# Optimization experiments

Measured on AMD Instinct MI355X. Metric: run time of the kernel, lower is better.

The kernel has to match this reference:

```python
import jax, jax.numpy as jnp
import numpy as np

FRAME_NUMBER = 1200

def _relgcn(x, W, rows, cols, vals, n_nodes):
    # Multi-relation sparse GCN: sum_r A_r @ (x @ W_r), then tanh.
    out = jnp.zeros((n_nodes, W.shape[-1]), dtype=x.dtype)
    for r in range(W.shape[0]):  # fixed small set of relations (5)
        xl = x @ W[r]                              # [N, D]
        msgs = vals[r][:, None] * xl[cols[r]]      # [E, D] gather
        out = out + jax.ops.segment_sum(msgs, rows[r], num_segments=n_nodes)
    return jnp.tanh(out)

def setup_inputs() -> dict:
    key = jax.random.key(0)
    ks = jax.random.split(key, 20)
    N, E, R, D, B, C = 11201, 100000, 5, 512, 32, 16
    s = lambda k, sh, sc=0.05: jax.random.normal(k, sh, dtype=jnp.float32) * sc
    return {
        "target_span": jax.random.normal(ks[0], (B, 4 * 512), dtype=jnp.float32),
        "frame_emb": s(ks[1], (FRAME_NUMBER + 1, D), 1.0),
        "role_emb": s(ks[2], (10001, D), 1.0),
        "rel_W0": s(ks[3], (R, D, D)),
        "rel_W1": s(ks[4], (R, D, D)),
        "span_W1": s(ks[5], (2048, 2048)),
        "span_b1": s(ks[6], (2048,)),
        "span_W2": s(ks[7], (2048, D)),
        "span_b2": s(ks[8], (D,)),
        "fp_W1": s(ks[9], (D, D)),
        "fp_b1": s(ks[10], (D,)),
        "fp_W2": s(ks[11], (D, D)),
        "fp_b2": s(ks[12], (D,)),
        "adj_vals": jax.random.uniform(ks[13], (R, E), dtype=jnp.float32),
        "fe_ids": jax.random.randint(ks[14], (10001,), 0, 10001),
        "adj_rows": jax.random.randint(ks[15], (R, E), 0, N),
        "adj_cols": jax.random.randint(ks[16], (R, E), 0, N),
        "gold_frame_id": jax.random.randint(ks[17], (B,), 0, C),
        "frame_list": jax.random.randint(ks[18], (B, C), 0, FRAME_NUMBER),
    }

def reference(target_span, frame_emb, role_emb, rel_W0, rel_W1,
              span_W1, span_b1, span_W2, span_b2,
              fp_W1, fp_b1, fp_W2, fp_b2, adj_vals,
              fe_ids, adj_rows, adj_cols, gold_frame_id, frame_list):
    B = target_span.shape[0]
    # Embedding lookups (frame_embedding(arange(frame_number)), role_embedding(fe_dict ids))
    all_frame = frame_emb[:FRAME_NUMBER]            # [1200, D]
    all_fe = role_emb[fe_ids]                       # [10001, D]
    x = jnp.concatenate([all_frame, all_fe], axis=0)  # [N, D]
    N = x.shape[0]
    # Two-layer multi-relation GCN over 5 sparse adjacencies
    x = _relgcn(x, rel_W0, adj_rows, adj_cols, adj_vals, N)
    all_embeddings = _relgcn(x, rel_W1, adj_rows, adj_cols, adj_vals, N)  # [N, D]
    # span_fc_layer Mlp: Linear(2048,2048) -> ReLU -> Linear(2048,512) (dropout in eval = identity)
    target_node = jax.nn.relu(target_span @ span_W1 + span_b1) @ span_W2 + span_b2  # [B, D]
    # frame_pred = RoleClassification: Linear -> ReLU -> Linear -> Tanh, then bmm with all node embeddings
    Q = jnp.tanh(jax.nn.relu(target_node @ fp_W1 + fp_b1) @ fp_W2 + fp_b2)          # [B, D]
    pred_frame_weight = jnp.einsum("nd,bd->bn", all_embeddings, Q)[:, :FRAME_NUMBER]  # [B, 1200]
    # gold frame path: one-hot select gold frame id from candidates, gather its node embedding
    gold_frame_label = jnp.take_along_axis(frame_list, gold_frame_id[:, None], axis=1)[:, 0]  # [B]
    frame_node = all_embeddings[gold_frame_label]   # [B, D] (embed_dropout in eval = identity)
    return jnp.concatenate([pred_frame_weight, frame_node], axis=-1)  # [B, 1200+512]
```

## Files before the change

kernel.cpp:

```cpp
#include <hip/hip_runtime.h>
#include <hip/hip_bf16.h>
#include <stdint.h>

typedef unsigned short u16;
typedef __attribute__((ext_vector_type(8))) short short8;
typedef __attribute__((ext_vector_type(4))) float float4v;

#define NNODES 11201
#define MPAD   11264
#define EEDGES 100000
#define RREL   5
#define DDIM   512
#define XLW    2560
#define FRAMES 1200
#define OUTC   1712

__device__ __forceinline__ float bf2f(u16 h) {
    return __uint_as_float(((uint32_t)h) << 16);
}
__device__ __forceinline__ u16 f2bf(float f) {
    uint32_t x = __float_as_uint(f);
    x += 0x7fffu + ((x >> 16) & 1u);
    return (u16)(x >> 16);
}
__device__ __forceinline__ float fast_tanh(float v) {
    v = fminf(fmaxf(v, -10.f), 10.f);
    float ex = __expf(2.f * v);
    return (ex - 1.f) / (ex + 1.f);
}

__global__ void hist_k(const int* __restrict__ rows, int* __restrict__ counts) {
    int tid = blockIdx.x * 256 + threadIdx.x;
    if (tid >= RREL * EEDGES) return;
    int r = tid / EEDGES;
    atomicAdd(&counts[r * NNODES + rows[tid]], 1);
}

__global__ __launch_bounds__(1024) void scan_offsets(const int* __restrict__ counts,
                                                     int* __restrict__ offs) {
    int r = blockIdx.x;
    const int* c = counts + (size_t)r * NNODES;
    int* o = offs + (size_t)r * (NNODES + 1);
    __shared__ int wsum[16];
    __shared__ int carry_s;
    const int lane = threadIdx.x & 63, wid = threadIdx.x >> 6;
    if (threadIdx.x == 0) carry_s = 0;
    __syncthreads();
    for (int base = 0; base < NNODES; base += 1024) {
        int idx = base + threadIdx.x;
        int orig = (idx < NNODES) ? c[idx] : 0;
        int v = orig;
        #pragma unroll
        for (int d = 1; d < 64; d <<= 1) {
            int t = __shfl_up(v, d, 64);
            if (lane >= d) v += t;
        }
        if (lane == 63) wsum[wid] = v;
        __syncthreads();
        if (wid == 0) {
            int wv = (lane < 16) ? wsum[lane] : 0;
            #pragma unroll
            for (int d = 1; d < 16; d <<= 1) {
                int t = __shfl_up(wv, d, 64);
                if (lane >= d) wv += t;
            }
            if (lane < 16) wsum[lane] = wv;
        }
        __syncthreads();
        int incl = carry_s + ((wid > 0) ? wsum[wid - 1] : 0) + v;
        if (idx < NNODES) o[idx] = incl - orig;
        __syncthreads();
        if (threadIdx.x == 1023) carry_s = incl;
    }
    __syncthreads();
    if (threadIdx.x == 0) o[NNODES] = carry_s;
}

__global__ void cursor_init(const int* __restrict__ offs, int* __restrict__ cursor) {
    int i = blockIdx.x * 256 + threadIdx.x;
    if (i >= RREL * NNODES) return;
    int r = i / NNODES, n = i - r * NNODES;
    cursor[i] = offs[r * (NNODES + 1) + n];
}

__global__ void scatter_k(const int* __restrict__ rows, const int* __restrict__ cols,
                          const float* __restrict__ vals, int* __restrict__ cursor,
                          int* __restrict__ colS, float* __restrict__ valS) {
    int tid = blockIdx.x * 256 + threadIdx.x;
    if (tid >= RREL * EEDGES) return;
    int r = tid / EEDGES;
    int row = rows[tid];
    int pos = atomicAdd(&cursor[r * NNODES + row], 1);
    colS[(size_t)r * EEDGES + pos] = cols[tid];
    valS[(size_t)r * EEDGES + pos] = vals[tid];
}

__global__ void build_x(const float* __restrict__ frame_emb, const float* __restrict__ role_emb,
                        const int* __restrict__ fe_ids, u16* __restrict__ x) {
    int t = blockIdx.x * 256 + threadIdx.x;
    int row = t >> 7, c4 = (t & 127) << 2;
    if (row >= NNODES) return;
    const float* src = (row < FRAMES) ? (frame_emb + (size_t)row * DDIM)
                                      : (role_emb + (size_t)fe_ids[row - FRAMES] * DDIM);
    float4 v = *(const float4*)(src + c4);
    ushort4 o = { f2bf(v.x), f2bf(v.y), f2bf(v.z), f2bf(v.w) };
    *(ushort4*)(x + (size_t)row * DDIM + c4) = o;
}

__global__ void build_tsp(const float* __restrict__ ts, u16* __restrict__ tsp) {
    int t = blockIdx.x * 256 + threadIdx.x;
    int row = t >> 9, c4 = (t & 511) << 2;
    ushort4 o = {0, 0, 0, 0};
    if (row < 32) {
        float4 v = *(const float4*)(ts + (size_t)row * 2048 + c4);
        o = ushort4{ f2bf(v.x), f2bf(v.y), f2bf(v.z), f2bf(v.w) };
    }
    *(ushort4*)(tsp + (size_t)row * 2048 + c4) = o;
}

__global__ void transpose_f2b(const float* __restrict__ in, u16* __restrict__ out,
                              int rows, int cols, int ldOut) {
    __shared__ u16 tile[32][33];
    in += (size_t)blockIdx.z * rows * cols;
    const size_t zoff = (size_t)blockIdx.z * rows;
    int c0 = blockIdx.x * 32, r0 = blockIdx.y * 32;
    int tx = threadIdx.x & 31, ty = threadIdx.x >> 5;
    #pragma unroll
    for (int i = 0; i < 4; ++i) {
        int rr = ty + i * 8;
        tile[rr][tx] = f2bf(in[(size_t)(r0 + rr) * cols + c0 + tx]);
    }
    __syncthreads();
    #pragma unroll
    for (int i = 0; i < 4; ++i) {
        int rr = ty + i * 8;
        out[(size_t)(c0 + rr) * ldOut + zoff + r0 + tx] = tile[tx][rr];
    }
}

template<int EPI, bool FOUT>
__global__ __launch_bounds__(256)
void gemm_bt(const u16* __restrict__ A, const u16* __restrict__ Bt,
             void* __restrict__ Cv, const float* __restrict__ bias,
             int K, int lda, int ldb, int ldc, int mGuard, int nGuard)
{
    __shared__ u16 As[128 * 32];
    __shared__ u16 Bs[128 * 32];
    const int tid = threadIdx.x;
    const int wave = tid >> 6, lane = tid & 63;
    const int m0 = blockIdx.y * 128, n0 = blockIdx.x * 128;
    const int srow = lane >> 2;
    const int skoff = (lane & 3) << 3;
    const int fr = lane & 15, quad = lane >> 4;
    const int wm = (wave & 1) << 6, wn = (wave >> 1) << 6;
    float4v acc[4][4] = {};

    for (int k0 = 0; k0 < K; k0 += 32) {
        #pragma unroll
        for (int i = 0; i < 2; ++i) {
            const int rb = (wave + i * 4) << 4;
            const u16* ga = A  + (size_t)(m0 + rb + srow) * lda + (k0 + skoff);
            const u16* gb = Bt + (size_t)(n0 + rb + srow) * ldb + (k0 + skoff);
            __builtin_amdgcn_global_load_lds(
                (const __attribute__((address_space(1))) unsigned int*)ga,
                (__attribute__((address_space(3))) unsigned int*)(As + rb * 32), 16, 0, 0);
            __builtin_amdgcn_global_load_lds(
                (const __attribute__((address_space(1))) unsigned int*)gb,
                (__attribute__((address_space(3))) unsigned int*)(Bs + rb * 32), 16, 0, 0);
        }
        __syncthreads();
        short8 a[4], b[4];
        #pragma unroll
        for (int t = 0; t < 4; ++t)
            a[t] = *(const short8*)(As + ((wm + t * 16 + fr) << 5) + (quad << 3));
        #pragma unroll
        for (int t = 0; t < 4; ++t)
            b[t] = *(const short8*)(Bs + ((wn + t * 16 + fr) << 5) + (quad << 3));
        #pragma unroll
        for (int i = 0; i < 4; ++i)
            #pragma unroll
            for (int j = 0; j < 4; ++j)
                acc[i][j] = __builtin_amdgcn_mfma_f32_16x16x32_bf16(a[i], b[j], acc[i][j], 0, 0, 0);
        __syncthreads();
    }

    #pragma unroll
    for (int i = 0; i < 4; ++i) {
        #pragma unroll
        for (int j = 0; j < 4; ++j) {
            const int n = n0 + wn + j * 16 + fr;
            float bv = 0.f;
            if (EPI == 1 || EPI == 2 || EPI == 3) { if (n < nGuard) bv = bias[n]; }
            #pragma unroll
            for (int rg = 0; rg < 4; ++rg) {
                const int m = m0 + wm + i * 16 + (quad << 2) + rg;
                if (m < mGuard && n < nGuard) {
                    float v = acc[i][j][rg];
                    if (EPI == 1 || EPI == 2 || EPI == 3) v += bv;
                    if (EPI == 1) v = fmaxf(v, 0.f);
                    if (EPI == 3 || EPI == 4) v = fast_tanh(v);
                    if (FOUT) ((float*)Cv)[(size_t)m * ldc + n] = v;
                    else      ((u16*)Cv)[(size_t)m * ldc + n] = f2bf(v);
                }
            }
        }
    }
}

__global__ __launch_bounds__(256)
void gemm_bt_sk(const u16* __restrict__ A, const u16* __restrict__ Bt,
                float* __restrict__ Cf, int K, int Kc, int lda, int ldb, int ldc)
{
    __shared__ u16 As[128 * 32];
    __shared__ u16 Bs[128 * 32];
    const int tid = threadIdx.x;
    const int wave = tid >> 6, lane = tid & 63;
    const int m0 = blockIdx.y * 128, n0 = blockIdx.x * 128;
    const int kb = blockIdx.z * Kc;
    const int ke = (kb + Kc < K) ? (kb + Kc) : K;
    const int srow = lane >> 2;
    const int skoff = (lane & 3) << 3;
    const int fr = lane & 15, quad = lane >> 4;
    const int wm = (wave & 1) << 6, wn = (wave >> 1) << 6;
    float4v acc[4][4] = {};

    for (int k0 = kb; k0 < ke; k0 += 32) {
        #pragma unroll
        for (int i = 0; i < 2; ++i) {
            const int rb = (wave + i * 4) << 4;
            const u16* ga = A  + (size_t)(m0 + rb + srow) * lda + (k0 + skoff);
            const u16* gb = Bt + (size_t)(n0 + rb + srow) * ldb + (k0 + skoff);
            __builtin_amdgcn_global_load_lds(
                (const __attribute__((address_space(1))) unsigned int*)ga,
                (__attribute__((address_space(3))) unsigned int*)(As + rb * 32), 16, 0, 0);
            __builtin_amdgcn_global_load_lds(
                (const __attribute__((address_space(1))) unsigned int*)gb,
                (__attribute__((address_space(3))) unsigned int*)(Bs + rb * 32), 16, 0, 0);
        }
        __syncthreads();
        short8 a[4], b[4];
        #pragma unroll
        for (int t = 0; t < 4; ++t)
            a[t] = *(const short8*)(As + ((wm + t * 16 + fr) << 5) + (quad << 3));
        #pragma unroll
        for (int t = 0; t < 4; ++t)
            b[t] = *(const short8*)(Bs + ((wn + t * 16 + fr) << 5) + (quad << 3));
        #pragma unroll
        for (int i = 0; i < 4; ++i)
            #pragma unroll
            for (int j = 0; j < 4; ++j)
                acc[i][j] = __builtin_amdgcn_mfma_f32_16x16x32_bf16(a[i], b[j], acc[i][j], 0, 0, 0);
        __syncthreads();
    }

    #pragma unroll
    for (int i = 0; i < 4; ++i)
        #pragma unroll
        for (int j = 0; j < 4; ++j) {
            const int n = n0 + wn + j * 16 + fr;
            #pragma unroll
            for (int rg = 0; rg < 4; ++rg) {
                const int m = m0 + wm + i * 16 + (quad << 2) + rg;
                atomicAdd(&Cf[(size_t)m * ldc + n], acc[i][j][rg]);
            }
        }
}

template<int ACT>
__global__ void sk_ep(const float* __restrict__ Cf, const float* __restrict__ bias,
                      u16* __restrict__ outp, int Ncols) {
    int t = blockIdx.x * 256 + threadIdx.x;
    if (t >= 128 * Ncols / 4) return;
    int i = t << 2;
    int col = i & (Ncols - 1);
    float4 v = *(const float4*)(Cf + i);
    v.x += bias[col]; v.y += bias[col + 1]; v.z += bias[col + 2]; v.w += bias[col + 3];
    if (ACT == 1) { v.x = fmaxf(v.x, 0.f); v.y = fmaxf(v.y, 0.f);
                    v.z = fmaxf(v.z, 0.f); v.w = fmaxf(v.w, 0.f); }
    if (ACT == 3) { v.x = fast_tanh(v.x); v.y = fast_tanh(v.y);
                    v.z = fast_tanh(v.z); v.w = fast_tanh(v.w); }
    ushort4 o = { f2bf(v.x), f2bf(v.y), f2bf(v.z), f2bf(v.w) };
    *(ushort4*)(outp + i) = o;
}

__device__ __forceinline__ void fma8(float* acc, uint4 u, float val) {
    acc[0] = fmaf(val, __uint_as_float(u.x << 16), acc[0]);
    acc[1] = fmaf(val, __uint_as_float(u.x & 0xffff0000u), acc[1]);
    acc[2] = fmaf(val, __uint_as_float(u.y << 16), acc[2]);
    acc[3] = fmaf(val, __uint_as_float(u.y & 0xffff0000u), acc[3]);
    acc[4] = fmaf(val, __uint_as_float(u.z << 16), acc[4]);
    acc[5] = fmaf(val, __uint_as_float(u.z & 0xffff0000u), acc[5]);
    acc[6] = fmaf(val, __uint_as_float(u.w << 16), acc[6]);
    acc[7] = fmaf(val, __uint_as_float(u.w & 0xffff0000u), acc[7]);
}

__global__ __launch_bounds__(256)
void spmm_agg(const u16* __restrict__ x, const int* __restrict__ offs,
              const int* __restrict__ colS, const float* __restrict__ valS,
              u16* __restrict__ agg)
{
    const int wave = threadIdx.x >> 6, lane = threadIdx.x & 63;
    const int n = blockIdx.x * 4 + wave;
    if (n >= NNODES) return;
    const u16* xr = x + (lane << 3);
    #pragma unroll
    for (int r = 0; r < RREL; ++r) {
        int s = offs[r * (NNODES + 1) + n];
        const int e = offs[r * (NNODES + 1) + n + 1];
        const int*   cp = colS + (size_t)r * EEDGES;
        const float* vp = valS + (size_t)r * EEDGES;
        float acc[8] = {0.f, 0.f, 0.f, 0.f, 0.f, 0.f, 0.f, 0.f};
        for (; s + 4 <= e; s += 4) {
            int   c0 = cp[s], c1 = cp[s + 1], c2 = cp[s + 2], c3 = cp[s + 3];
            float v0 = vp[s], v1 = vp[s + 1], v2 = vp[s + 2], v3 = vp[s + 3];
            uint4 u0 = *(const uint4*)(xr + (size_t)c0 * DDIM);
            uint4 u1 = *(const uint4*)(xr + (size_t)c1 * DDIM);
            uint4 u2 = *(const uint4*)(xr + (size_t)c2 * DDIM);
            uint4 u3 = *(const uint4*)(xr + (size_t)c3 * DDIM);
            fma8(acc, u0, v0); fma8(acc, u1, v1); fma8(acc, u2, v2); fma8(acc, u3, v3);
        }
        for (; s < e; ++s) {
            int col = cp[s];
            float val = vp[s];
            uint4 u = *(const uint4*)(xr + (size_t)col * DDIM);
            fma8(acc, u, val);
        }
        uint4 o;
        o.x = (uint32_t)f2bf(acc[0]) | ((uint32_t)f2bf(acc[1]) << 16);
        o.y = (uint32_t)f2bf(acc[2]) | ((uint32_t)f2bf(acc[3]) << 16);
        o.z = (uint32_t)f2bf(acc[4]) | ((uint32_t)f2bf(acc[5]) << 16);
        o.w = (uint32_t)f2bf(acc[6]) | ((uint32_t)f2bf(acc[7]) << 16);
        *(uint4*)(agg + (size_t)n * XLW + (r << 9) + (lane << 3)) = o;
    }
}

__global__ void frame_gather(const u16* __restrict__ emb, const int* __restrict__ frame_list,
                             const int* __restrict__ gold, float* __restrict__ out) {
    int t = blockIdx.x * 256 + threadIdx.x;
    if (t >= 32 * 64) return;
    int b = t >> 6, lane = t & 63;
    int label = frame_list[b * 16 + gold[b]];
    const u16* src = emb + (size_t)label * DDIM + (lane << 3);
    float* dst = out + (size_t)b * OUTC + FRAMES + (lane << 3);
    float4 o0 = { bf2f(src[0]), bf2f(src[1]), bf2f(src[2]), bf2f(src[3]) };
    float4 o1 = { bf2f(src[4]), bf2f(src[5]), bf2f(src[6]), bf2f(src[7]) };
    *(float4*)(dst) = o0;
    *(float4*)(dst + 4) = o1;
}

extern "C" void kernel_launch(void* const* d_in, const int* in_sizes, int n_in,
                              void* d_out, int out_size, void* d_ws, size_t ws_size,
                              hipStream_t stream) {
    const float* target_span = (const float*)d_in[0];
    const float* frame_emb   = (const float*)d_in[1];
    const float* role_emb    = (const float*)d_in[2];
    const float* rel_W0      = (const float*)d_in[3];
    const float* rel_W1      = (const float*)d_in[4];
    const float* span_W1     = (const float*)d_in[5];
    const float* span_b1     = (const float*)d_in[6];
    const float* span_W2     = (const float*)d_in[7];
    const float* span_b2     = (const float*)d_in[8];
    const float* fp_W1       = (const float*)d_in[9];
    const float* fp_b1       = (const float*)d_in[10];
    const float* fp_W2       = (const float*)d_in[11];
    const float* fp_b2       = (const float*)d_in[12];
    const float* adj_vals    = (const float*)d_in[13];
    const int* fe_ids      = (const int*)d_in[14];
    const int* adj_rows    = (const int*)d_in[15];
    const int* adj_cols    = (const int*)d_in[16];
    const int* gold_id     = (const int*)d_in[17];
    const int* frame_list  = (const int*)d_in[18];
    float* out = (float*)d_out;

    char* ws = (char*)d_ws;
    size_t off = 0;
    auto take = [&](size_t bytes) -> char* {
        char* p = ws + off;
        off = (off + bytes + 255) & ~(size_t)255;
        return p;
    };
    u16* x      = (u16*)take((size_t)MPAD * DDIM * 2);
    u16* agg    = (u16*)take((size_t)MPAD * XLW * 2);
    u16* w0t    = (u16*)take((size_t)512 * XLW * 2);
    u16* w1t    = (u16*)take((size_t)512 * XLW * 2);
    u16* s1t    = (u16*)take((size_t)2048 * 2048 * 2);
    u16* s2t    = (u16*)take((size_t)512 * 2048 * 2);
    u16* f1t    = (u16*)take((size_t)512 * 512 * 2);
    u16* f2t    = (u16*)take((size_t)512 * 512 * 2);
    int* counts = (int*)take((size_t)RREL * NNODES * 4);
    int* offs   = (int*)take((size_t)RREL * (NNODES + 1) * 4);
    int* cursor = (int*)take((size_t)RREL * NNODES * 4);
    int* colS   = (int*)take((size_t)RREL * EEDGES * 4);
    float* valS = (float*)take((size_t)RREL * EEDGES * 4);
    u16* tsp    = (u16*)take((size_t)128 * 2048 * 2);
    u16* h1     = (u16*)take((size_t)128 * 2048 * 2);
    u16* tn     = (u16*)take((size_t)128 * 512 * 2);
    u16* h2     = (u16*)take((size_t)128 * 512 * 2);
    u16* Qb     = (u16*)take((size_t)128 * 512 * 2);
    float* CfAll = (float*)take((size_t)(128 * 2048 + 3 * 128 * 512) * 4);
    float* Cf1 = CfAll;
    float* Cf2 = Cf1 + 128 * 2048;
    float* Cf3 = Cf2 + 128 * 512;
    float* Cf4 = Cf3 + 128 * 512;

    hipMemsetAsync(counts, 0, (size_t)RREL * NNODES * 4, stream);
    hipMemsetAsync(CfAll, 0, (size_t)(128 * 2048 + 3 * 128 * 512) * 4, stream);

    hist_k<<<(RREL * EEDGES + 255) / 256, 256, 0, stream>>>(adj_rows, counts);
    scan_offsets<<<RREL, 1024, 0, stream>>>(counts, offs);
    cursor_init<<<(RREL * NNODES + 255) / 256, 256, 0, stream>>>(offs, cursor);
    scatter_k<<<(RREL * EEDGES + 255) / 256, 256, 0, stream>>>(adj_rows, adj_cols, adj_vals,
                                                               cursor, colS, valS);
    build_x<<<(NNODES * 128 + 255) / 256, 256, 0, stream>>>(frame_emb, role_emb, fe_ids, x);
    build_tsp<<<256, 256, 0, stream>>>(target_span, tsp);

    transpose_f2b<<<dim3(16, 16, RREL), 256, 0, stream>>>(rel_W0, w0t, 512, 512, XLW);
    transpose_f2b<<<dim3(16, 16, RREL), 256, 0, stream>>>(rel_W1, w1t, 512, 512, XLW);
    transpose_f2b<<<dim3(64, 64, 1), 256, 0, stream>>>(span_W1, s1t, 2048, 2048, 2048);
    transpose_f2b<<<dim3(16, 64, 1), 256, 0, stream>>>(span_W2, s2t, 2048, 512, 2048);
    transpose_f2b<<<dim3(16, 16, 1), 256, 0, stream>>>(fp_W1, f1t, 512, 512, 512);
    transpose_f2b<<<dim3(16, 16, 1), 256, 0, stream>>>(fp_W2, f2t, 512, 512, 512);

    spmm_agg<<<(NNODES + 3) / 4, 256, 0, stream>>>(x, offs, colS, valS, agg);
    gemm_bt<4, false><<<dim3(4, MPAD / 128), 256, 0, stream>>>(
        agg, w0t, x, nullptr, XLW, XLW, XLW, 512, NNODES, 512);
    spmm_agg<<<(NNODES + 3) / 4, 256, 0, stream>>>(x, offs, colS, valS, agg);
    gemm_bt<4, false><<<dim3(4, MPAD / 128), 256, 0, stream>>>(
        agg, w1t, x, nullptr, XLW, XLW, XLW, 512, NNODES, 512);

    gemm_bt_sk<<<dim3(16, 1, 8), 256, 0, stream>>>(tsp, s1t, Cf1, 2048, 256, 2048, 2048, 2048);
    sk_ep<1><<<(128 * 2048 / 4 + 255) / 256, 256, 0, stream>>>(Cf1, span_b1, h1, 2048);
    gemm_bt_sk<<<dim3(4, 1, 8), 256, 0, stream>>>(h1, s2t, Cf2, 2048, 256, 2048, 2048, 512);
    sk_ep<2><<<(128 * 512 / 4 + 255) / 256, 256, 0, stream>>>(Cf2, span_b2, tn, 512);
    gemm_bt_sk<<<dim3(4, 1, 4), 256, 0, stream>>>(tn, f1t, Cf3, 512, 128, 512, 512, 512);
    sk_ep<1><<<(128 * 512 / 4 + 255) / 256, 256, 0, stream>>>(Cf3, fp_b1, h2, 512);
    gemm_bt_sk<<<dim3(4, 1, 4), 256, 0, stream>>>(h2, f2t, Cf4, 512, 128, 512, 512, 512);
    sk_ep<3><<<(128 * 512 / 4 + 255) / 256, 256, 0, stream>>>(Cf4, fp_b2, Qb, 512);

    gemm_bt<0, true><<<dim3((FRAMES + 127) / 128, 1), 256, 0, stream>>>(
        Qb, x, out, nullptr, 512, 512, 512, OUTC, 32, FRAMES);
    frame_gather<<<8, 256, 0, stream>>>(x, frame_list, gold_id, out);
}
```

Baseline: 546.2 us.

## Split-K the GCN GEMMs, swizzle LDS reads, and merge small prep kernels

The two large GCN GEMMs (M=11264, K=2560) now use split-K over 5 slices, accumulating with atomics into an fp32 buffer followed by a separate tanh epilogue pass. The final prediction GEMM is also split-K. The LDS load offsets are XOR-swizzled to reduce bank conflicts, and the offset scan now computes each relation in a single pass and writes the cursors directly. The embedding, span, and weight conversion kernels are merged into two launches. In exchange, this adds a 23MB fp32 buffer with extra memsets and an epilogue pass per layer, and float atomics make the accumulation order nondeterministic.

```diff
diff --git a/kernel.cpp b/kernel.cpp
--- a/kernel.cpp
+++ b/kernel.cpp
@@ -37,50 +37,50 @@
 }
 
 __global__ __launch_bounds__(1024) void scan_offsets(const int* __restrict__ counts,
-                                                     int* __restrict__ offs) {
+                                                     int* __restrict__ offs,
+                                                     int* __restrict__ cursor) {
+    const int PER = 11;
     int r = blockIdx.x;
     const int* c = counts + (size_t)r * NNODES;
     int* o = offs + (size_t)r * (NNODES + 1);
+    int* cur = cursor + (size_t)r * NNODES;
     __shared__ int wsum[16];
-    __shared__ int carry_s;
     const int lane = threadIdx.x & 63, wid = threadIdx.x >> 6;
-    if (threadIdx.x == 0) carry_s = 0;
+    int base = threadIdx.x * PER;
+    int v[PER];
+    int s = 0;
+    #pragma unroll
+    for (int t = 0; t < PER; ++t) {
+        int idx = base + t;
+        v[t] = (idx < NNODES) ? c[idx] : 0;
+        s += v[t];
+    }
+    int incl = s;
+    #pragma unroll
+    for (int d = 1; d < 64; d <<= 1) {
+        int t = __shfl_up(incl, d, 64);
+        if (lane >= d) incl += t;
+    }
+    if (lane == 63) wsum[wid] = incl;
     __syncthreads();
-    for (int base = 0; base < NNODES; base += 1024) {
-        int idx = base + threadIdx.x;
-        int orig = (idx < NNODES) ? c[idx] : 0;
-        int v = orig;
-        #pragma unroll
-        for (int d = 1; d < 64; d <<= 1) {
-            int t = __shfl_up(v, d, 64);
-            if (lane >= d) v += t;
-        }
-        if (lane == 63) wsum[wid] = v;
-        __syncthreads();
-        if (wid == 0) {
-            int wv = (lane < 16) ? wsum[lane] : 0;
-            #pragma unroll
-            for (int d = 1; d < 16; d <<= 1) {
-                int t = __shfl_up(wv, d, 64);
-                if (lane >= d) wv += t;
-            }
-            if (lane < 16) wsum[lane] = wv;
-        }
-        __syncthreads();
-        int incl = carry_s + ((wid > 0) ? wsum[wid - 1] : 0) + v;
-        if (idx < NNODES) o[idx] = incl - orig;
-        __syncthreads();
-        if (threadIdx.x == 1023) carry_s = incl;
+    if (wid == 0) {
+        int wv = (lane < 16) ? wsum[lane] : 0;
+        #pragma unroll
+        for (int d = 1; d < 16; d <<= 1) {
+            int t = __shfl_up(wv, d, 64);
+            if (lane >= d) wv += t;
+        }
+        if (lane < 16) wsum[lane] = wv;
     }
     __syncthreads();
-    if (threadIdx.x == 0) o[NNODES] = carry_s;
-}
-
-__global__ void cursor_init(const int* __restrict__ offs, int* __restrict__ cursor) {
-    int i = blockIdx.x * 256 + threadIdx.x;
-    if (i >= RREL * NNODES) return;
-    int r = i / NNODES, n = i - r * NNODES;
-    cursor[i] = offs[r * (NNODES + 1) + n];
+    int run = incl - s + ((wid > 0) ? wsum[wid - 1] : 0);
+    #pragma unroll
+    for (int t = 0; t < PER; ++t) {
+        int idx = base + t;
+        if (idx < NNODES) { o[idx] = run; cur[idx] = run; }
+        run += v[t];
+    }
+    if (threadIdx.x == 1023) o[NNODES] = run;
 }
 
 __global__ void scatter_k(const int* __restrict__ rows, const int* __restrict__ cols,
@@ -95,67 +95,109 @@
     valS[(size_t)r * EEDGES + pos] = vals[tid];
 }
 
-__global__ void build_x(const float* __restrict__ frame_emb, const float* __restrict__ role_emb,
-                        const int* __restrict__ fe_ids, u16* __restrict__ x) {
-    int t = blockIdx.x * 256 + threadIdx.x;
-    int row = t >> 7, c4 = (t & 127) << 2;
-    if (row >= NNODES) return;
-    const float* src = (row < FRAMES) ? (frame_emb + (size_t)row * DDIM)
-                                      : (role_emb + (size_t)fe_ids[row - FRAMES] * DDIM);
-    float4 v = *(const float4*)(src + c4);
-    ushort4 o = { f2bf(v.x), f2bf(v.y), f2bf(v.z), f2bf(v.w) };
-    *(ushort4*)(x + (size_t)row * DDIM + c4) = o;
-}
-
-__global__ void build_tsp(const float* __restrict__ ts, u16* __restrict__ tsp) {
-    int t = blockIdx.x * 256 + threadIdx.x;
-    int row = t >> 9, c4 = (t & 511) << 2;
-    ushort4 o = {0, 0, 0, 0};
-    if (row < 32) {
-        float4 v = *(const float4*)(ts + (size_t)row * 2048 + c4);
-        o = ushort4{ f2bf(v.x), f2bf(v.y), f2bf(v.z), f2bf(v.w) };
-    }
-    *(ushort4*)(tsp + (size_t)row * 2048 + c4) = o;
-}
-
-__global__ void transpose_f2b(const float* __restrict__ in, u16* __restrict__ out,
-                              int rows, int cols, int ldOut) {
+#define BX_BLOCKS 5601
+__global__ void prep_inputs(const float* __restrict__ frame_emb,
+                            const float* __restrict__ role_emb,
+                            const int* __restrict__ fe_ids,
+                            const float* __restrict__ ts,
+                            u16* __restrict__ x, u16* __restrict__ tsp) {
+    int bid = blockIdx.x;
+    if (bid < BX_BLOCKS) {
+        int t = bid * 256 + threadIdx.x;
+        int row = t >> 7, c4 = (t & 127) << 2;
+        if (row >= NNODES) return;
+        const float* src = (row < FRAMES) ? (frame_emb + (size_t)row * DDIM)
+                                          : (role_emb + (size_t)fe_ids[row - FRAMES] * DDIM);
+        float4 v = *(const float4*)(src + c4);
+        ushort4 o = { f2bf(v.x), f2bf(v.y), f2bf(v.z), f2bf(v.w) };
+        *(ushort4*)(x + (size_t)row * DDIM + c4) = o;
+    } else {
+        int t = (bid - BX_BLOCKS) * 256 + threadIdx.x;
+        int row = t >> 9, c4 = (t & 511) << 2;
+        ushort4 o = {0, 0, 0, 0};
+        if (row < 32) {
+            float4 v = *(const float4*)(ts + (size_t)row * 2048 + c4);
+            o = ushort4{ f2bf(v.x), f2bf(v.y), f2bf(v.z), f2bf(v.w) };
+        }
+        *(ushort4*)(tsp + (size_t)row * 2048 + c4) = o;
+    }
+}
+
+__global__ void transpose_all(const float* __restrict__ w0, const float* __restrict__ w1,
+                              const float* __restrict__ s1, const float* __restrict__ s2,
+                              const float* __restrict__ f1, const float* __restrict__ f2,
+                              u16* __restrict__ w0t, u16* __restrict__ w1t,
+                              u16* __restrict__ s1t, u16* __restrict__ s2t,
+                              u16* __restrict__ f1t, u16* __restrict__ f2t) {
+    int b = blockIdx.x;
+    const float* src; u16* dst;
+    int cols, ldOut, bx, by;
+    size_t zcol = 0;
+    if (b < 1280) {
+        int rel = b >> 8, rem = b & 255;
+        src = w0 + (size_t)rel * 262144; dst = w0t;
+        cols = 512; ldOut = XLW; zcol = (size_t)rel * 512;
+        bx = rem & 15; by = rem >> 4;
+    } else if (b < 2560) {
+        b -= 1280;
+        int rel = b >> 8, rem = b & 255;
+        src = w1 + (size_t)rel * 262144; dst = w1t;
+        cols = 512; ldOut = XLW; zcol = (size_t)rel * 512;
+        bx = rem & 15; by = rem >> 4;
+    } else if (b < 6656) {
+        b -= 2560;
+        src = s1; dst = s1t; cols = 2048; ldOut = 2048;
+        bx = b & 63; by = b >> 6;
+    } else if (b < 7680) {
+        b -= 6656;
+        src = s2; dst = s2t; cols = 512; ldOut = 2048;
+        bx = b & 15; by = b >> 4;
+    } else if (b < 7936) {
+        b -= 7680;
+        src = f1; dst = f1t; cols = 512; ldOut = 512;
+        bx = b & 15; by = b >> 4;
+    } else {
+        b -= 7936;
+        src = f2; dst = f2t; cols = 512; ldOut = 512;
+        bx = b & 15; by = b >> 4;
+    }
     __shared__ u16 tile[32][33];
-    in += (size_t)blockIdx.z * rows * cols;
-    const size_t zoff = (size_t)blockIdx.z * rows;
-    int c0 = blockIdx.x * 32, r0 = blockIdx.y * 32;
+    int c0 = bx * 32, r0 = by * 32;
     int tx = threadIdx.x & 31, ty = threadIdx.x >> 5;
     #pragma unroll
     for (int i = 0; i < 4; ++i) {
         int rr = ty + i * 8;
-        tile[rr][tx] = f2bf(in[(size_t)(r0 + rr) * cols + c0 + tx]);
+        tile[rr][tx] = f2bf(src[(size_t)(r0 + rr) * cols + c0 + tx]);
     }
     __syncthreads();
     #pragma unroll
     for (int i = 0; i < 4; ++i) {
         int rr = ty + i * 8;
-        out[(size_t)(c0 + rr) * ldOut + zoff + r0 + tx] = tile[tx][rr];
-    }
-}
-
-template<int EPI, bool FOUT>
+        dst[(size_t)(c0 + rr) * ldOut + zcol + r0 + tx] = tile[tx][rr];
+    }
+}
+
+template<bool GUARDM>
 __global__ __launch_bounds__(256)
-void gemm_bt(const u16* __restrict__ A, const u16* __restrict__ Bt,
-             void* __restrict__ Cv, const float* __restrict__ bias,
-             int K, int lda, int ldb, int ldc, int mGuard, int nGuard)
+void gemm_sk(const u16* __restrict__ A, const u16* __restrict__ Bt,
+             float* __restrict__ Cf, int K, int Kc,
+             int lda, int ldb, int ldc, int mGuard)
 {
     __shared__ u16 As[128 * 32];
     __shared__ u16 Bs[128 * 32];
     const int tid = threadIdx.x;
     const int wave = tid >> 6, lane = tid & 63;
     const int m0 = blockIdx.y * 128, n0 = blockIdx.x * 128;
+    const int kb = blockIdx.z * Kc;
     const int srow = lane >> 2;
-    const int skoff = (lane & 3) << 3;
+    const int schunk = ((lane & 3) - (lane >> 4)) & 3;
+    const int skoff = schunk << 3;
     const int fr = lane & 15, quad = lane >> 4;
+    const int pa = ((quad + (fr >> 2)) & 3) << 3;
     const int wm = (wave & 1) << 6, wn = (wave >> 1) << 6;
     float4v acc[4][4] = {};
 
-    for (int k0 = 0; k0 < K; k0 += 32) {
+    for (int k0 = kb; k0 < kb + Kc; k0 += 32) {
         #pragma unroll
         for (int i = 0; i < 2; ++i) {
             const int rb = (wave + i * 4) << 4;
@@ -172,10 +214,10 @@
         short8 a[4], b[4];
         #pragma unroll
         for (int t = 0; t < 4; ++t)
-            a[t] = *(const short8*)(As + ((wm + t * 16 + fr) << 5) + (quad << 3));
+            a[t] = *(const short8*)(As + ((wm + t * 16 + fr) << 5) + pa);
         #pragma unroll
         for (int t = 0; t < 4; ++t)
-            b[t] = *(const short8*)(Bs + ((wn + t * 16 + fr) << 5) + (quad << 3));
+            b[t] = *(const short8*)(Bs + ((wn + t * 16 + fr) << 5) + pa);
         #pragma unroll
         for (int i = 0; i < 4; ++i)
             #pragma unroll
@@ -185,75 +227,6 @@
     }
 
     #pragma unroll
-    for (int i = 0; i < 4; ++i) {
-        #pragma unroll
-        for (int j = 0; j < 4; ++j) {
-            const int n = n0 + wn + j * 16 + fr;
-            float bv = 0.f;
-            if (EPI == 1 || EPI == 2 || EPI == 3) { if (n < nGuard) bv = bias[n]; }
-            #pragma unroll
-            for (int rg = 0; rg < 4; ++rg) {
-                const int m = m0 + wm + i * 16 + (quad << 2) + rg;
-                if (m < mGuard && n < nGuard) {
-                    float v = acc[i][j][rg];
-                    if (EPI == 1 || EPI == 2 || EPI == 3) v += bv;
-                    if (EPI == 1) v = fmaxf(v, 0.f);
-                    if (EPI == 3 || EPI == 4) v = fast_tanh(v);
-                    if (FOUT) ((float*)Cv)[(size_t)m * ldc + n] = v;
-                    else      ((u16*)Cv)[(size_t)m * ldc + n] = f2bf(v);
-                }
-            }
-        }
-    }
-}
-
-__global__ __launch_bounds__(256)
-void gemm_bt_sk(const u16* __restrict__ A, const u16* __restrict__ Bt,
-                float* __restrict__ Cf, int K, int Kc, int lda, int ldb, int ldc)
-{
-    __shared__ u16 As[128 * 32];
-    __shared__ u16 Bs[128 * 32];
-    const int tid = threadIdx.x;
-    const int wave = tid >> 6, lane = tid & 63;
-    const int m0 = blockIdx.y * 128, n0 = blockIdx.x * 128;
-    const int kb = blockIdx.z * Kc;
-    const int ke = (kb + Kc < K) ? (kb + Kc) : K;
-    const int srow = lane >> 2;
-    const int skoff = (lane & 3) << 3;
-    const int fr = lane & 15, quad = lane >> 4;
-    const int wm = (wave & 1) << 6, wn = (wave >> 1) << 6;
-    float4v acc[4][4] = {};
-
-    for (int k0 = kb; k0 < ke; k0 += 32) {
-        #pragma unroll
-        for (int i = 0; i < 2; ++i) {
-            const int rb = (wave + i * 4) << 4;
-            const u16* ga = A  + (size_t)(m0 + rb + srow) * lda + (k0 + skoff);
-            const u16* gb = Bt + (size_t)(n0 + rb + srow) * ldb + (k0 + skoff);
-            __builtin_amdgcn_global_load_lds(
-                (const __attribute__((address_space(1))) unsigned int*)ga,
-                (__attribute__((address_space(3))) unsigned int*)(As + rb * 32), 16, 0, 0);
-            __builtin_amdgcn_global_load_lds(
-                (const __attribute__((address_space(1))) unsigned int*)gb,
-                (__attribute__((address_space(3))) unsigned int*)(Bs + rb * 32), 16, 0, 0);
-        }
-        __syncthreads();
-        short8 a[4], b[4];
-        #pragma unroll
-        for (int t = 0; t < 4; ++t)
-            a[t] = *(const short8*)(As + ((wm + t * 16 + fr) << 5) + (quad << 3));
-        #pragma unroll
-        for (int t = 0; t < 4; ++t)
-            b[t] = *(const short8*)(Bs + ((wn + t * 16 + fr) << 5) + (quad << 3));
-        #pragma unroll
-        for (int i = 0; i < 4; ++i)
-            #pragma unroll
-            for (int j = 0; j < 4; ++j)
-                acc[i][j] = __builtin_amdgcn_mfma_f32_16x16x32_bf16(a[i], b[j], acc[i][j], 0, 0, 0);
-        __syncthreads();
-    }
-
-    #pragma unroll
     for (int i = 0; i < 4; ++i)
         #pragma unroll
         for (int j = 0; j < 4; ++j) {
@@ -261,20 +234,23 @@
             #pragma unroll
             for (int rg = 0; rg < 4; ++rg) {
                 const int m = m0 + wm + i * 16 + (quad << 2) + rg;
-                atomicAdd(&Cf[(size_t)m * ldc + n], acc[i][j][rg]);
+                if (!GUARDM || m < mGuard)
+                    atomicAdd(&Cf[(size_t)m * ldc + n], acc[i][j][rg]);
             }
         }
 }
 
-template<int ACT>
+template<int ACT, bool HASB>
 __global__ void sk_ep(const float* __restrict__ Cf, const float* __restrict__ bias,
-                      u16* __restrict__ outp, int Ncols) {
+                      u16* __restrict__ outp, int Ncols, int total4) {
     int t = blockIdx.x * 256 + threadIdx.x;
-    if (t >= 128 * Ncols / 4) return;
+    if (t >= total4) return;
     int i = t << 2;
-    int col = i & (Ncols - 1);
     float4 v = *(const float4*)(Cf + i);
-    v.x += bias[col]; v.y += bias[col + 1]; v.z += bias[col + 2]; v.w += bias[col + 3];
+    if (HASB) {
+        int col = i & (Ncols - 1);
+        v.x += bias[col]; v.y += bias[col + 1]; v.z += bias[col + 2]; v.w += bias[col + 3];
+    }
     if (ACT == 1) { v.x = fmaxf(v.x, 0.f); v.y = fmaxf(v.y, 0.f);
                     v.z = fmaxf(v.z, 0.f); v.w = fmaxf(v.w, 0.f); }
     if (ACT == 3) { v.x = fast_tanh(v.x); v.y = fast_tanh(v.y);
@@ -381,6 +357,7 @@
     };
     u16* x      = (u16*)take((size_t)MPAD * DDIM * 2);
     u16* agg    = (u16*)take((size_t)MPAD * XLW * 2);
+    float* C32  = (float*)take((size_t)MPAD * DDIM * 4);
     u16* w0t    = (u16*)take((size_t)512 * XLW * 2);
     u16* w1t    = (u16*)take((size_t)512 * XLW * 2);
     u16* s1t    = (u16*)take((size_t)2048 * 2048 * 2);
@@ -404,40 +381,41 @@
     float* Cf4 = Cf3 + 128 * 512;
 
     hipMemsetAsync(counts, 0, (size_t)RREL * NNODES * 4, stream);
+    hipMemsetAsync(C32, 0, (size_t)MPAD * DDIM * 4, stream);
     hipMemsetAsync(CfAll, 0, (size_t)(128 * 2048 + 3 * 128 * 512) * 4, stream);
+    hipMemsetAsync(out, 0, (size_t)32 * OUTC * 4, stream);
 
     hist_k<<<(RREL * EEDGES + 255) / 256, 256, 0, stream>>>(adj_rows, counts);
-    scan_offsets<<<RREL, 1024, 0, stream>>>(counts, offs);
-    cursor_init<<<(RREL * NNODES + 255) / 256, 256, 0, stream>>>(offs, cursor);
+    scan_offsets<<<RREL, 1024, 0, stream>>>(counts, offs, cursor);
     scatter_k<<<(RREL * EEDGES + 255) / 256, 256, 0, stream>>>(adj_rows, adj_cols, adj_vals,
                                                                cursor, colS, valS);
-    build_x<<<(NNODES * 128 + 255) / 256, 256, 0, stream>>>(frame_emb, role_emb, fe_ids, x);
-    build_tsp<<<256, 256, 0, stream>>>(target_span, tsp);
-
-    transpose_f2b<<<dim3(16, 16, RREL), 256, 0, stream>>>(rel_W0, w0t, 512, 512, XLW);
-    transpose_f2b<<<dim3(16, 16, RREL), 256, 0, stream>>>(rel_W1, w1t, 512, 512, XLW);
-    transpose_f2b<<<dim3(64, 64, 1), 256, 0, stream>>>(span_W1, s1t, 2048, 2048, 2048);
-    transpose_f2b<<<dim3(16, 64, 1), 256, 0, stream>>>(span_W2, s2t, 2048, 512, 2048);
-    transpose_f2b<<<dim3(16, 16, 1), 256, 0, stream>>>(fp_W1, f1t, 512, 512, 512);
-    transpose_f2b<<<dim3(16, 16, 1), 256, 0, stream>>>(fp_W2, f2t, 512, 512, 512);
+    prep_inputs<<<BX_BLOCKS + 256, 256, 0, stream>>>(frame_emb, role_emb, fe_ids,
+                                                     target_span, x, tsp);
+    transpose_all<<<8192, 256, 0, stream>>>(rel_W0, rel_W1, span_W1, span_W2, fp_W1, fp_W2,
+                                            w0t, w1t, s1t, s2t, f1t, f2t);
 
     spmm_agg<<<(NNODES + 3) / 4, 256, 0, stream>>>(x, offs, colS, valS, agg);
-    gemm_bt<4, false><<<dim3(4, MPAD / 128), 256, 0, stream>>>(
-        agg, w0t, x, nullptr, XLW, XLW, XLW, 512, NNODES, 512);
+    gemm_sk<false><<<dim3(4, MPAD / 128, 5), 256, 0, stream>>>(
+        agg, w0t, C32, XLW, 512, XLW, XLW, 512, MPAD);
+    sk_ep<3, false><<<(MPAD * 512 / 4 + 255) / 256, 256, 0, stream>>>(
+        C32, nullptr, x, 512, MPAD * 512 / 4);
+    hipMemsetAsync(C32, 0, (size_t)MPAD * DDIM * 4, stream);
     spmm_agg<<<(NNODES + 3) / 4, 256, 0, stream>>>(x, offs, colS, valS, agg);
-    gemm_bt<4, false><<<dim3(4, MPAD / 128), 256, 0, stream>>>(
-        agg, w1t, x, nullptr, XLW, XLW, XLW, 512, NNODES, 512);
-
-    gemm_bt_sk<<<dim3(16, 1, 8), 256, 0, stream>>>(tsp, s1t, Cf1, 2048, 256, 2048, 2048, 2048);
-    sk_ep<1><<<(128 * 2048 / 4 + 255) / 256, 256, 0, stream>>>(Cf1, span_b1, h1, 2048);
-    gemm_bt_sk<<<dim3(4, 1, 8), 256, 0, stream>>>(h1, s2t, Cf2, 2048, 256, 2048, 2048, 512);
-    sk_ep<2><<<(128 * 512 / 4 + 255) / 256, 256, 0, stream>>>(Cf2, span_b2, tn, 512);
-    gemm_bt_sk<<<dim3(4, 1, 4), 256, 0, stream>>>(tn, f1t, Cf3, 512, 128, 512, 512, 512);
-    sk_ep<1><<<(128 * 512 / 4 + 255) / 256, 256, 0, stream>>>(Cf3, fp_b1, h2, 512);
-    gemm_bt_sk<<<dim3(4, 1, 4), 256, 0, stream>>>(h2, f2t, Cf4, 512, 128, 512, 512, 512);
-    sk_ep<3><<<(128 * 512 / 4 + 255) / 256, 256, 0, stream>>>(Cf4, fp_b2, Qb, 512);
-
-    gemm_bt<0, true><<<dim3((FRAMES + 127) / 128, 1), 256, 0, stream>>>(
-        Qb, x, out, nullptr, 512, 512, 512, OUTC, 32, FRAMES);
+    gemm_sk<false><<<dim3(4, MPAD / 128, 5), 256, 0, stream>>>(
+        agg, w1t, C32, XLW, 512, XLW, XLW, 512, MPAD);
+    sk_ep<3, false><<<(MPAD * 512 / 4 + 255) / 256, 256, 0, stream>>>(
+        C32, nullptr, x, 512, MPAD * 512 / 4);
+
+    gemm_sk<false><<<dim3(16, 1, 8), 256, 0, stream>>>(tsp, s1t, Cf1, 2048, 256, 2048, 2048, 2048, 128);
+    sk_ep<1, true><<<(128 * 2048 / 4 + 255) / 256, 256, 0, stream>>>(Cf1, span_b1, h1, 2048, 128 * 2048 / 4);
+    gemm_sk<false><<<dim3(4, 1, 8), 256, 0, stream>>>(h1, s2t, Cf2, 2048, 256, 2048, 2048, 512, 128);
+    sk_ep<0, true><<<(128 * 512 / 4 + 255) / 256, 256, 0, stream>>>(Cf2, span_b2, tn, 512, 128 * 512 / 4);
+    gemm_sk<false><<<dim3(4, 1, 4), 256, 0, stream>>>(tn, f1t, Cf3, 512, 128, 512, 512, 512, 128);
+    sk_ep<1, true><<<(128 * 512 / 4 + 255) / 256, 256, 0, stream>>>(Cf3, fp_b1, h2, 512, 128 * 512 / 4);
+    gemm_sk<false><<<dim3(4, 1, 4), 256, 0, stream>>>(h2, f2t, Cf4, 512, 128, 512, 512, 512, 128);
+    sk_ep<3, true><<<(128 * 512 / 4 + 255) / 256, 256, 0, stream>>>(Cf4, fp_b2, Qb, 512, 128 * 512 / 4);
+
+    gemm_sk<true><<<dim3((FRAMES + 127) / 128, 1, 4), 256, 0, stream>>>(
+        Qb, x, out, 512, 128, 512, 512, OUTC, 32);
     frame_gather<<<8, 256, 0, stream>>>(x, frame_list, gold_id, out);
 }
```

After: 628.3 us. 1.15x slower.
